# Kernel tuning notes

Hardware: AMD Instinct MI355X
Metric: run time of the kernel (lower is better)

## Reference

```python
import jax, jax.numpy as jnp
import numpy as np

IOU_THRESHOLD = 0.5  # default iou_threshold of nms/class_spec_nms


def _nms_keep_mask(boxes, scores, iou_threshold):
    """Faithful port of the hand-rolled greedy NMS.

    The torch version builds a variable-length index list; here we return the
    equivalent fixed-shape boolean keep mask over the N boxes (jit-friendly).
    """
    n = scores.shape[0]
    x1, y1, x2, y2 = boxes[:, 0], boxes[:, 1], boxes[:, 2], boxes[:, 3]
    areas = (x2 - x1) * (y2 - y1)                       # [N]
    # pairwise intersection via broadcasted min/max (same math as the matmul-
    # with-ones trick in the source, without materializing the ones matrices)
    xi = jnp.minimum(x2[:, None], x2[None, :]) - jnp.maximum(x1[:, None], x1[None, :])
    yi = jnp.minimum(y2[:, None], y2[None, :]) - jnp.maximum(y1[:, None], y1[None, :])
    inter = jnp.maximum(xi, 0.0) * jnp.maximum(yi, 0.0)  # [N,N]
    iou = inter / (areas[:, None] + areas[None, :] - inter)

    first_max = scores.max()
    first_min = scores.min()
    curr_idx0 = jnp.argmax(scores)

    # carry: (candidate mask, working scores copy, keep mask, curr max, curr idx)
    init = (scores < first_max, scores, jnp.zeros((n,), dtype=bool), first_max, curr_idx0)

    def cond(state):
        mask, _, _, cmax, _ = state
        return jnp.any(mask) & (cmax >= first_min)

    def body(state):
        mask, sc, keep, cmax, cidx = state
        mask = mask & (iou[cidx] <= iou_threshold)   # suppress overlaps with current max
        mask = mask.at[cidx].set(False)
        keep = keep.at[cidx].set(True)               # keep current max
        sc = jnp.where(mask, sc, first_min - 1.0)    # kill suppressed scores
        cidx = jnp.argmax(sc)
        return mask, sc, keep, sc[cidx], cidx

    _, _, keep, _, _ = jax.lax.while_loop(cond, body, init)
    return keep


def setup_inputs() -> dict:
    key = jax.random.key(0)
    k1, k2, k3, k4, k5, k6 = jax.random.split(key, 6)
    N = 4096    # pre-NMS candidate boxes
    L = 16384   # p3 locations for a 1024x1024 image at stride 8 (128*128)
    xy = jax.random.uniform(k1, (N, 2), dtype=jnp.float32) * 900.0
    wh = jax.random.uniform(k2, (N, 2), dtype=jnp.float32) * 100.0 + 1.0
    boxes = jnp.concatenate([xy, xy + wh], axis=1)          # valid x1<x2, y1<y2
    scores = jax.random.uniform(k3, (N,), dtype=jnp.float32)
    class_ids = jax.random.randint(k4, (N,), 0, 80, dtype=jnp.int32)
    locations = jax.random.uniform(k5, (L, 2), dtype=jnp.float32) * 1024.0
    deltas = jax.random.uniform(k6, (L, 4), dtype=jnp.float32)  # positive gt deltas
    return {"boxes": boxes, "scores": scores, "class_ids": class_ids,
            "locations": locations, "deltas": deltas, "stride": 8}


def reference(boxes, scores, class_ids, locations, deltas, stride):
    # ---- class_spec_nms: class-offset trick then plain NMS ----
    max_coordinate = boxes.max()
    offsets = class_ids.astype(boxes.dtype) * (max_coordinate + 1.0)
    boxes_for_nms = boxes + offsets[:, None]
    keep_mask = _nms_keep_mask(boxes_for_nms, scores, IOU_THRESHOLD)

    # ---- fcos_apply_deltas_to_locations ----
    clipped = jnp.maximum(deltas, 0.0)
    s = jnp.asarray(stride, dtype=deltas.dtype)
    px, py = locations[:, 0], locations[:, 1]
    pred_boxes = jnp.stack([px - clipped[:, 0] * s,
                            py - clipped[:, 1] * s,
                            px + clipped[:, 2] * s,
                            py + clipped[:, 3] * s], axis=1)  # [L,4]

    # ---- fcos_make_centerness_targets ----
    lr_min = jnp.minimum(deltas[:, 0], deltas[:, 2])
    tb_min = jnp.minimum(deltas[:, 1], deltas[:, 3])
    lr_max = jnp.maximum(deltas[:, 0], deltas[:, 2])
    tb_max = jnp.maximum(deltas[:, 1], deltas[:, 3])
    centerness = jnp.sqrt((lr_min * tb_min) / (lr_max * tb_max))
    centerness = jnp.where(jnp.all(deltas == -1.0, axis=1), -1.0, centerness)

    pred_out = jnp.concatenate([pred_boxes, centerness[:, None]], axis=1)  # [L,5]
    return keep_mask, pred_out
```

## Files before the change

kernel.cpp:

```cpp
#include <hip/hip_runtime.h>
#include <stdint.h>

#define NB 4096
#define NBLK 64
#define LLOC 16384
#define IOU_THR 0.5f
#define ECAP 1024
#define RANKB 256

typedef unsigned long long u64;

__device__ __forceinline__ u64 readlane64(u64 v, int lane) {
    unsigned lo = (unsigned)__builtin_amdgcn_readlane((int)(unsigned)(v & 0xffffffffull), lane);
    unsigned hi = (unsigned)__builtin_amdgcn_readlane((int)(unsigned)(v >> 32), lane);
    return ((u64)hi << 32) | (u64)lo;
}

__global__ void __launch_bounds__(256) fused_front(
        const float* __restrict__ boxes, const float* __restrict__ scores,
        const float* __restrict__ loc, const float* __restrict__ deltas,
        const int* __restrict__ stride_p,
        float* __restrict__ pred_out, float* __restrict__ maxc,
        int* __restrict__ sidx, int* __restrict__ counts) {
    __shared__ __align__(16) float sh[NB];
    __shared__ float red[4];
    int blk = blockIdx.x;
    int t = threadIdx.x;

    if (blk < 64) {
        int i = blk * 256 + t;
        float s = (float)stride_p[0];
        float2 p = ((const float2*)loc)[i];
        float4 d = ((const float4*)deltas)[i];
        float c0 = fmaxf(d.x, 0.f), c1 = fmaxf(d.y, 0.f);
        float c2 = fmaxf(d.z, 0.f), c3 = fmaxf(d.w, 0.f);
        float b0 = p.x - c0 * s;
        float b1 = p.y - c1 * s;
        float b2 = p.x + c2 * s;
        float b3 = p.y + c3 * s;
        float lr_min = fminf(d.x, d.z), tb_min = fminf(d.y, d.w);
        float lr_max = fmaxf(d.x, d.z), tb_max = fmaxf(d.y, d.w);
        float cent = sqrtf((lr_min * tb_min) / (lr_max * tb_max));
        if (d.x == -1.f && d.y == -1.f && d.z == -1.f && d.w == -1.f) cent = -1.f;
        float* o = pred_out + (size_t)i * 5;
        o[0] = b0; o[1] = b1; o[2] = b2; o[3] = b3; o[4] = cent;
    } else if (blk < 64 + RANKB) {
        for (int i = t; i < NB; i += 256) sh[i] = scores[i];
        __syncthreads();
        int wave = t >> 6, lane = t & 63;
        int base = (blk - 64) * 16 + wave * 4;
        float my0 = sh[base + 0], my1 = sh[base + 1];
        float my2 = sh[base + 2], my3 = sh[base + 3];
        int c0 = 0, c1 = 0, c2 = 0, c3 = 0;
#pragma unroll 8
        for (int k = 0; k < 64; ++k) {
            int j = lane + k * 64;
            float sj = sh[j];
            c0 += (sj > my0) || (sj == my0 && j < base + 0);
            c1 += (sj > my1) || (sj == my1 && j < base + 1);
            c2 += (sj > my2) || (sj == my2 && j < base + 2);
            c3 += (sj > my3) || (sj == my3 && j < base + 3);
        }
        for (int o = 32; o > 0; o >>= 1) {
            c0 += __shfl_down(c0, o); c1 += __shfl_down(c1, o);
            c2 += __shfl_down(c2, o); c3 += __shfl_down(c3, o);
        }
        if (lane == 0) {
            sidx[c0] = base + 0; sidx[c1] = base + 1;
            sidx[c2] = base + 2; sidx[c3] = base + 3;
        }
    } else {
        if (t < NBLK) counts[t] = 0;
        float m = -3.0e38f;
        for (int i = t; i < NB * 4; i += 256) m = fmaxf(m, boxes[i]);
        for (int o = 32; o > 0; o >>= 1) m = fmaxf(m, __shfl_down(m, o));
        if ((t & 63) == 0) red[t >> 6] = m;
        __syncthreads();
        if (t == 0) *maxc = fmaxf(fmaxf(red[0], red[1]), fmaxf(red[2], red[3]));
    }
}

__global__ void __launch_bounds__(256) prep_gather(
        const float* __restrict__ boxes, const int* __restrict__ cls,
        const float* __restrict__ maxc, const int* __restrict__ sidx,
        float* __restrict__ sboxes, float* __restrict__ sareas) {
    int i = blockIdx.x * 256 + threadIdx.x;
    if (i >= NB) return;
    int j = sidx[i];
    float off = (float)cls[j] * (maxc[0] + 1.0f);
    float4 b = ((const float4*)boxes)[j];
    b.x += off; b.y += off; b.z += off; b.w += off;
    ((float4*)sboxes)[i] = b;
    sareas[i] = (b.z - b.x) * (b.w - b.y);
}

__global__ void __launch_bounds__(64) edge_kernel(
        const float* __restrict__ sboxes, const float* __restrict__ sareas,
        int* __restrict__ counts, uint4* __restrict__ entries) {
    int c = blockIdx.x, r = blockIdx.y;
    if (c < r) return;
    __shared__ float4 cb[64];
    __shared__ float ca[64];
    int t = threadIdx.x;
    cb[t] = ((const float4*)sboxes)[c * 64 + t];
    ca[t] = sareas[c * 64 + t];
    __syncthreads();
    float4 rb = ((const float4*)sboxes)[r * 64 + t];
    float ra = sareas[r * 64 + t];
    u64 w = 0;
#pragma unroll 8
    for (int j = 0; j < 64; ++j) {
        float4 b = cb[j];
        float xi = fminf(rb.z, b.z) - fmaxf(rb.x, b.x);
        float yi = fminf(rb.w, b.w) - fmaxf(rb.y, b.y);
        float inter = fmaxf(xi, 0.f) * fmaxf(yi, 0.f);
        float iou = inter / (ra + ca[j] - inter);
        w |= (u64)(iou > IOU_THR) << j;
    }
    if (c == r) w &= ~(1ull << t);
    if (w) {
        int idx = atomicAdd(&counts[r], 1);
        if (idx < ECAP)
            entries[r * ECAP + idx] =
                make_uint4((unsigned)(t | (c << 8)), 0u,
                           (unsigned)(w & 0xffffffffull), (unsigned)(w >> 32));
    }
}

__global__ void __launch_bounds__(64) scan_kernel(
        const int* __restrict__ counts, const uint4* __restrict__ entries,
        const int* __restrict__ sidx, float* __restrict__ keep_out) {
    const int lane = threadIdx.x;
    int cnt_l = counts[lane];
    u64 accv = 0;
    u64 keptall = 0;
    u64 self = 1ull << lane;

    uint4 cur = entries[lane];
    for (int b = 0; b < NBLK; ++b) {
        uint4 nxt;
        if (b < NBLK - 1) nxt = entries[(b + 1) * ECAP + lane];

        int cnt = __builtin_amdgcn_readlane(cnt_l, b);
        if (cnt > ECAP) cnt = ECAP;
        int cfast = cnt < 64 ? cnt : 64;

        u64 colw = self;
        for (int e = 0; e < cfast; ++e) {
            unsigned meta = (unsigned)__builtin_amdgcn_readlane((int)cur.x, e);
            int l = meta & 255, c = meta >> 8;
            if (c == b) {
                unsigned lo = (unsigned)__builtin_amdgcn_readlane((int)cur.z, e);
                unsigned hi = (unsigned)__builtin_amdgcn_readlane((int)cur.w, e);
                if (lane == l) colw |= ((u64)hi << 32) | lo;
            }
        }
        for (int e = 64; e < cnt; ++e) {
            uint4 x = entries[b * ECAP + e];
            int l = x.x & 255, c = x.x >> 8;
            if (c == b && lane == l) colw |= ((u64)x.w << 32) | x.z;
        }

        u64 rem = readlane64(accv, b);
        u64 avail = ~rem;
        u64 edges = colw & avail & ~self;
        u64 involved = __ballot(edges != 0ull) & avail;
        u64 keptm = avail & ~involved;
        u64 sub = involved;
        while (sub) {
            int i = (int)__builtin_ctzll(sub);
            keptm |= 1ull << i;
            u64 ci = readlane64(colw, i);
            sub &= ~(ci | (1ull << i));
        }
        if (lane == b) keptall = keptm;

        for (int e = 0; e < cfast; ++e) {
            unsigned meta = (unsigned)__builtin_amdgcn_readlane((int)cur.x, e);
            unsigned lo   = (unsigned)__builtin_amdgcn_readlane((int)cur.z, e);
            unsigned hi   = (unsigned)__builtin_amdgcn_readlane((int)cur.w, e);
            int l = meta & 255, c = meta >> 8;
            if (((keptm >> l) & 1ull) && lane == c) accv |= ((u64)hi << 32) | lo;
        }
        for (int e = 64; e < cnt; ++e) {
            uint4 x = entries[b * ECAP + e];
            int l = x.x & 255, c = x.x >> 8;
            if (((keptm >> l) & 1ull) && lane == c) accv |= ((u64)x.w << 32) | x.z;
        }
        cur = nxt;
    }

#pragma unroll 8
    for (int bb = 0; bb < NBLK; ++bb) {
        u64 kw = readlane64(keptall, bb);
        int idx = sidx[bb * 64 + lane];
        keep_out[idx] = ((kw >> lane) & 1ull) ? 1.0f : 0.0f;
    }
}

extern "C" void kernel_launch(void* const* d_in, const int* in_sizes, int n_in,
                              void* d_out, int out_size, void* d_ws, size_t ws_size,
                              hipStream_t stream) {
    const float* boxes   = (const float*)d_in[0];
    const float* scores  = (const float*)d_in[1];
    const int*   cls     = (const int*)d_in[2];
    const float* loc     = (const float*)d_in[3];
    const float* deltas  = (const float*)d_in[4];
    const int*   stride  = (const int*)d_in[5];

    float* out = (float*)d_out;
    float* keep_out = out;
    float* pred_out = out + NB;

    char* ws = (char*)d_ws;
    float* maxc    = (float*)ws;                     ws += 16;
    int*   sidx    = (int*)ws;                       ws += NB * sizeof(int);
    float* sboxes  = (float*)ws;                     ws += NB * 4 * sizeof(float);
    float* sareas  = (float*)ws;                     ws += NB * sizeof(float);
    int*   counts  = (int*)ws;                       ws += NBLK * sizeof(int) + 16;
    uint4* entries = (uint4*)ws;

    fused_front<<<64 + RANKB + 1, 256, 0, stream>>>(boxes, scores, loc, deltas, stride,
                                                    pred_out, maxc, sidx, counts);
    prep_gather<<<NB / 256, 256, 0, stream>>>(boxes, cls, maxc, sidx, sboxes, sareas);
    edge_kernel<<<dim3(NBLK, NBLK), 64, 0, stream>>>(sboxes, sareas, counts, entries);
    scan_kernel<<<1, 64, 0, stream>>>(counts, entries, sidx, keep_out);
}
```

Baseline: 114.8 us.

## Fuse gather into edge kernel, launch triangular grid, deepen scan prefetch

```diff
diff --git a/kernel.cpp b/kernel.cpp
--- a/kernel.cpp
+++ b/kernel.cpp
@@ -7,6 +7,7 @@
 #define IOU_THR 0.5f
 #define ECAP 1024
 #define RANKB 256
+#define NTRI (NBLK * (NBLK + 1) / 2)
 
 typedef unsigned long long u64;
 
@@ -80,33 +81,36 @@
     }
 }
 
-__global__ void __launch_bounds__(256) prep_gather(
+__global__ void __launch_bounds__(64) edge_kernel(
         const float* __restrict__ boxes, const int* __restrict__ cls,
         const float* __restrict__ maxc, const int* __restrict__ sidx,
-        float* __restrict__ sboxes, float* __restrict__ sareas) {
-    int i = blockIdx.x * 256 + threadIdx.x;
-    if (i >= NB) return;
-    int j = sidx[i];
-    float off = (float)cls[j] * (maxc[0] + 1.0f);
-    float4 b = ((const float4*)boxes)[j];
-    b.x += off; b.y += off; b.z += off; b.w += off;
-    ((float4*)sboxes)[i] = b;
-    sareas[i] = (b.z - b.x) * (b.w - b.y);
-}
-
-__global__ void __launch_bounds__(64) edge_kernel(
-        const float* __restrict__ sboxes, const float* __restrict__ sareas,
         int* __restrict__ counts, uint4* __restrict__ entries) {
-    int c = blockIdx.x, r = blockIdx.y;
-    if (c < r) return;
+    int idx = blockIdx.x, r = 0;
+    while (idx >= NBLK - r) { idx -= NBLK - r; ++r; }
+    int c = r + idx;
+
     __shared__ float4 cb[64];
     __shared__ float ca[64];
     int t = threadIdx.x;
-    cb[t] = ((const float4*)sboxes)[c * 64 + t];
-    ca[t] = sareas[c * 64 + t];
+    float mc1 = maxc[0] + 1.0f;
+
+    int jr = sidx[r * 64 + t];
+    float offr = (float)cls[jr] * mc1;
+    float4 rb = ((const float4*)boxes)[jr];
+    rb.x += offr; rb.y += offr; rb.z += offr; rb.w += offr;
+    float ra = (rb.z - rb.x) * (rb.w - rb.y);
+
+    if (c == r) {
+        cb[t] = rb; ca[t] = ra;
+    } else {
+        int jc = sidx[c * 64 + t];
+        float offc = (float)cls[jc] * mc1;
+        float4 b = ((const float4*)boxes)[jc];
+        b.x += offc; b.y += offc; b.z += offc; b.w += offc;
+        cb[t] = b; ca[t] = (b.z - b.x) * (b.w - b.y);
+    }
     __syncthreads();
-    float4 rb = ((const float4*)sboxes)[r * 64 + t];
-    float ra = sareas[r * 64 + t];
+
     u64 w = 0;
 #pragma unroll 8
     for (int j = 0; j < 64; ++j) {
@@ -119,9 +123,9 @@
     }
     if (c == r) w &= ~(1ull << t);
     if (w) {
-        int idx = atomicAdd(&counts[r], 1);
-        if (idx < ECAP)
-            entries[r * ECAP + idx] =
+        int slot = atomicAdd(&counts[r], 1);
+        if (slot < ECAP)
+            entries[r * ECAP + slot] =
                 make_uint4((unsigned)(t | (c << 8)), 0u,
                            (unsigned)(w & 0xffffffffull), (unsigned)(w >> 32));
     }
@@ -137,9 +141,10 @@
     u64 self = 1ull << lane;
 
     uint4 cur = entries[lane];
+    uint4 n1  = entries[ECAP + lane];
     for (int b = 0; b < NBLK; ++b) {
-        uint4 nxt;
-        if (b < NBLK - 1) nxt = entries[(b + 1) * ECAP + lane];
+        uint4 n2;
+        if (b < NBLK - 2) n2 = entries[(u64)(b + 2) * ECAP + lane];
 
         int cnt = __builtin_amdgcn_readlane(cnt_l, b);
         if (cnt > ECAP) cnt = ECAP;
@@ -156,7 +161,7 @@
             }
         }
         for (int e = 64; e < cnt; ++e) {
-            uint4 x = entries[b * ECAP + e];
+            uint4 x = entries[(u64)b * ECAP + e];
             int l = x.x & 255, c = x.x >> 8;
             if (c == b && lane == l) colw |= ((u64)x.w << 32) | x.z;
         }
@@ -183,11 +188,11 @@
             if (((keptm >> l) & 1ull) && lane == c) accv |= ((u64)hi << 32) | lo;
         }
         for (int e = 64; e < cnt; ++e) {
-            uint4 x = entries[b * ECAP + e];
+            uint4 x = entries[(u64)b * ECAP + e];
             int l = x.x & 255, c = x.x >> 8;
             if (((keptm >> l) & 1ull) && lane == c) accv |= ((u64)x.w << 32) | x.z;
         }
-        cur = nxt;
+        cur = n1; n1 = n2;
     }
 
 #pragma unroll 8
@@ -215,14 +220,11 @@
     char* ws = (char*)d_ws;
     float* maxc    = (float*)ws;                     ws += 16;
     int*   sidx    = (int*)ws;                       ws += NB * sizeof(int);
-    float* sboxes  = (float*)ws;                     ws += NB * 4 * sizeof(float);
-    float* sareas  = (float*)ws;                     ws += NB * sizeof(float);
     int*   counts  = (int*)ws;                       ws += NBLK * sizeof(int) + 16;
     uint4* entries = (uint4*)ws;
 
     fused_front<<<64 + RANKB + 1, 256, 0, stream>>>(boxes, scores, loc, deltas, stride,
                                                     pred_out, maxc, sidx, counts);
-    prep_gather<<<NB / 256, 256, 0, stream>>>(boxes, cls, maxc, sidx, sboxes, sareas);
-    edge_kernel<<<dim3(NBLK, NBLK), 64, 0, stream>>>(sboxes, sareas, counts, entries);
+    edge_kernel<<<NTRI, 64, 0, stream>>>(boxes, cls, maxc, sidx, counts, entries);
     scan_kernel<<<1, 64, 0, stream>>>(counts, entries, sidx, keep_out);
 }
```

Result: faster. 103.8 us (-9.5%).
